# Performance work log

Hardware: AMD Instinct MI355X
Metric: run time of the kernel (lower is better)

The kernel has to match this reference:

```python
import jax, jax.numpy as jnp
import numpy as np

DIM = 1024
N_HEADS = 16
B, S = 2, 2048


def setup_inputs() -> dict:
    key = jax.random.key(0)
    ks = jax.random.split(key, 5)
    scale = 1.0 / np.sqrt(DIM)
    x = jax.random.normal(ks[0], (B, S, DIM), dtype=jnp.float32)
    mask = jax.random.randint(ks[1], (B, S), 0, 2, dtype=jnp.int32)
    Wq = jax.random.normal(ks[2], (DIM, DIM), dtype=jnp.float32) * scale
    Wk = jax.random.normal(ks[3], (DIM, DIM), dtype=jnp.float32) * scale
    Wv = jax.random.normal(ks[4], (DIM, DIM), dtype=jnp.float32) * scale
    bq = jnp.zeros((DIM,), jnp.float32)
    bk = jnp.zeros((DIM,), jnp.float32)
    bv = jnp.zeros((DIM,), jnp.float32)
    return {"x": x, "mask": mask, "Wq": Wq, "bq": bq, "Wk": Wk, "bk": bk, "Wv": Wv, "bv": bv}


def reference(x, mask, Wq, bq, Wk, bk, Wv, bv):
    # x: (B,S,D); project to q,k,v then split heads: (B,H,S,Dh)
    H = N_HEADS
    Bn, Sn, D = x.shape
    Dh = D // H

    def heads(t):
        return t.reshape(Bn, Sn, H, Dh).transpose(0, 2, 1, 3)

    q = heads(x @ Wq + bq)
    k = heads(x @ Wk + bk)
    v = heads(x @ Wv + bv)

    scores = jnp.einsum("bhsd,bhtd->bhst", q, k) / jnp.sqrt(jnp.float32(Dh))
    m = mask.astype(jnp.float32)[:, None, None, :]  # (B,1,1,S)
    scores = scores - 10000.0 * (1.0 - m)
    attn = jax.nn.softmax(scores, axis=-1)  # dropout is identity at eval (p=0)
    h = jnp.einsum("bhst,bhtd->bhsd", attn, v)
    return h.transpose(0, 2, 1, 3).reshape(Bn, Sn, D)
```

## Files before the change

### kernel.cpp

```cpp
#include <hip/hip_runtime.h>
#include <math.h>

#define DIMD 1024
#define NH 16
#define DH 64
#define BB 2
#define SS 2048
#define M_TOTAL (BB * SS)

typedef _Float16 half8 __attribute__((ext_vector_type(8)));
typedef _Float16 half4v __attribute__((ext_vector_type(4)));
typedef __fp16 fp16x2 __attribute__((ext_vector_type(2)));
typedef float floatx4 __attribute__((ext_vector_type(4)));
typedef float floatx16 __attribute__((ext_vector_type(16)));

#define QSCALE 0.18033688011112042f

__device__ __forceinline__ void load16_to_lds(const void* g, void* l) {
    __builtin_amdgcn_global_load_lds(
        (const __attribute__((address_space(1))) void*)g,
        (__attribute__((address_space(3))) void*)l, 16, 0, 0);
}

__device__ __forceinline__ unsigned pkh(float a, float b) {
    union { fp16x2 h; unsigned u; } c;
    c.h = __builtin_amdgcn_cvt_pkrtz(a, b);
    return c.u;
}

__global__ __launch_bounds__(256) void prep_kernel(
    const float* __restrict__ x,
    const float* __restrict__ Wq, const float* __restrict__ Wk,
    const float* __restrict__ Wv, const int* __restrict__ mask,
    _Float16* __restrict__ xh, _Float16* __restrict__ Wt,
    int* __restrict__ pos, int* __restrict__ nvalid)
{
    __shared__ _Float16 Ls[64][74];
    __shared__ int cnt[32], off[32];
    const int bid = blockIdx.x, tid = threadIdx.x;

    if (bid < 1024) {
#pragma unroll
        for (int j = 0; j < 4; ++j) {
            const int i = j * 262144 + bid * 256 + tid;
            float4 v = ((const float4*)x)[i];
            half4v hv = {(_Float16)v.x, (_Float16)v.y, (_Float16)v.z, (_Float16)v.w};
            *(half4v*)&xh[(size_t)i * 4] = hv;
        }
    } else if (bid < 1792) {
        const int wid = bid - 1024;
        const int z = wid >> 8, rem = wid & 255;
        const float* W = z == 0 ? Wq : (z == 1 ? Wk : Wv);
        _Float16* o = Wt + (size_t)z * DIMD * DIMD;
        const int k0 = (rem >> 4) * 64, n0 = (rem & 15) * 64;

#pragma unroll
        for (int it = 0; it < 4; ++it) {
            const int k = it * 16 + (tid >> 4);
            const int n4 = (tid & 15) * 4;
            float4 v = *(const float4*)&W[(size_t)(k0 + k) * DIMD + n0 + n4];
            Ls[k][n4 + 0] = (_Float16)v.x;
            Ls[k][n4 + 1] = (_Float16)v.y;
            Ls[k][n4 + 2] = (_Float16)v.z;
            Ls[k][n4 + 3] = (_Float16)v.w;
        }
        __syncthreads();
#pragma unroll
        for (int it = 0; it < 2; ++it) {
            const int idx = it * 256 + tid;
            const int n = idx >> 3, kc = idx & 7;
            union { _Float16 h[8]; uint4 u4; } t;
#pragma unroll
            for (int j = 0; j < 8; ++j) t.h[j] = Ls[kc * 8 + j][n];
            *(uint4*)&o[(size_t)(n0 + n) * DIMD + k0 + kc * 8] = t.u4;
        }
    } else {
        const int b = bid - 1792;
        const int wv = tid >> 6, lane = tid & 63;
        const unsigned long long lanemask = (lane == 63)
            ? 0x7fffffffffffffffull : ((1ull << lane) - 1ull);
        unsigned long long bms[8];
#pragma unroll
        for (int cc = 0; cc < 8; ++cc) {
            const int c = wv * 8 + cc;
            const int mv = mask[b * SS + c * 64 + lane];
            bms[cc] = __ballot(mv != 0);
            if (lane == 0) cnt[c] = __popcll(bms[cc]);
        }
        __syncthreads();
        if (tid == 0) {
            int s = 0;
            for (int c = 0; c < 32; ++c) { off[c] = s; s += cnt[c]; }
            nvalid[b] = s;
        }
        __syncthreads();
#pragma unroll
        for (int cc = 0; cc < 8; ++cc) {
            const int c = wv * 8 + cc;
            const int valid = (int)((bms[cc] >> lane) & 1ull);
            pos[b * SS + c * 64 + lane] =
                valid ? (off[c] + __popcll(bms[cc] & lanemask)) : -1;
        }
    }
}

__global__ __launch_bounds__(256) void proj_gemm(
    const _Float16* __restrict__ xh, const _Float16* __restrict__ Wt,
    const float* __restrict__ bq, const float* __restrict__ bk,
    const float* __restrict__ bv, const int* __restrict__ pos,
    _Float16* __restrict__ Q, _Float16* __restrict__ K, _Float16* __restrict__ Vt)
{
    const int z = blockIdx.z;
    const float* bias = z == 0 ? bq : (z == 1 ? bk : bv);
    const _Float16* Wz = Wt + (size_t)z * DIMD * DIMD;

    const _Float16* Aptr; const _Float16* Bptr; int m0, n0;
    if (z == 2) { Aptr = Wz; Bptr = xh; m0 = blockIdx.y * 128; n0 = blockIdx.x * 128; }
    else        { Aptr = xh; Bptr = Wz; m0 = blockIdx.x * 128; n0 = blockIdx.y * 128; }

    __shared__ _Float16 Ah[128 * 64];
    __shared__ _Float16 Bh[128 * 64];

    const int tid = threadIdx.x;
    const int wave = tid >> 6, lane = tid & 63;
    const int quad = lane >> 4, l16 = lane & 15;
    const int wm = (wave >> 1) * 64, wn = (wave & 1) * 64;
    const int sw = l16 & 7;

    const int tid8 = tid >> 3;
    const int gc = (tid & 7) ^ (tid8 & 7);
    const _Float16* ap = Aptr + (size_t)(m0 + tid8) * DIMD + gc * 8;
    const _Float16* bp = Bptr + (size_t)(n0 + tid8) * DIMD + gc * 8;
    const size_t RS = (size_t)32 * DIMD;
    _Float16* AhW = &Ah[(size_t)tid * 8];
    _Float16* BhW = &Bh[(size_t)tid * 8];

    floatx4 acc[4][4];
#pragma unroll
    for (int i = 0; i < 4; ++i)
#pragma unroll
        for (int j = 0; j < 4; ++j) acc[i][j] = (floatx4){0.f, 0.f, 0.f, 0.f};

    uint4 a0, a1, a2, a3, b0, b1, b2, b3;
    a0 = *(const uint4*)(ap);
    a1 = *(const uint4*)(ap + RS);
    a2 = *(const uint4*)(ap + 2 * RS);
    a3 = *(const uint4*)(ap + 3 * RS);
    b0 = *(const uint4*)(bp);
    b1 = *(const uint4*)(bp + RS);
    b2 = *(const uint4*)(bp + 2 * RS);
    b3 = *(const uint4*)(bp + 3 * RS);

    for (int kt = 0; kt < 16; ++kt) {
        *(uint4*)(AhW)        = a0;
        *(uint4*)(AhW + 2048) = a1;
        *(uint4*)(AhW + 4096) = a2;
        *(uint4*)(AhW + 6144) = a3;
        *(uint4*)(BhW)        = b0;
        *(uint4*)(BhW + 2048) = b1;
        *(uint4*)(BhW + 4096) = b2;
        *(uint4*)(BhW + 6144) = b3;

        if (kt < 15) {
            const _Float16* apk = ap + (kt + 1) * 64;
            const _Float16* bpk = bp + (kt + 1) * 64;
            a0 = *(const uint4*)(apk);
            a1 = *(const uint4*)(apk + RS);
            a2 = *(const uint4*)(apk + 2 * RS);
            a3 = *(const uint4*)(apk + 3 * RS);
            b0 = *(const uint4*)(bpk);
            b1 = *(const uint4*)(bpk + RS);
            b2 = *(const uint4*)(bpk + 2 * RS);
            b3 = *(const uint4*)(bpk + 3 * RS);
        }

        __syncthreads();

#pragma unroll
        for (int kc = 0; kc < 2; ++kc) {
            const int coff = ((quad + kc * 4) ^ sw) * 8;
            half8 af[4], bf[4];
#pragma unroll
            for (int mt = 0; mt < 4; ++mt)
                af[mt] = *(const half8*)&Ah[(wm + mt * 16 + l16) * 64 + coff];
#pragma unroll
            for (int nt = 0; nt < 4; ++nt)
                bf[nt] = *(const half8*)&Bh[(wn + nt * 16 + l16) * 64 + coff];
#pragma unroll
            for (int mt = 0; mt < 4; ++mt)
#pragma unroll
                for (int nt = 0; nt < 4; ++nt)
                    acc[mt][nt] = __builtin_amdgcn_mfma_f32_16x16x32_f16(
                        af[mt], bf[nt], acc[mt][nt], 0, 0, 0);
        }

        __syncthreads();
    }

    if (z < 2) {
        int prr[4][4];
#pragma unroll
        for (int mt = 0; mt < 4; ++mt)
#pragma unroll
            for (int r = 0; r < 4; ++r) {
                const int m = m0 + wm + mt * 16 + quad * 4 + r;
                prr[mt][r] = (z == 0) ? (m & 2047) : pos[m];
            }
#pragma unroll
        for (int nt = 0; nt < 4; ++nt) {
            const int n = n0 + wn + nt * 16 + l16;
            const float bn = bias[n];
            const int h = n >> 6, d = n & 63;
#pragma unroll
            for (int mt = 0; mt < 4; ++mt) {
#pragma unroll
                for (int r = 0; r < 4; ++r) {
                    if (prr[mt][r] < 0) continue;
                    const int m = m0 + wm + mt * 16 + quad * 4 + r;
                    const int b = m >> 11;
                    const _Float16 val = (_Float16)((acc[mt][nt][r] + bn) *
                                                    (z == 0 ? QSCALE : 1.0f));
                    _Float16* dst = (z == 0) ? Q : K;
                    dst[((((size_t)b * NH + h) * SS + prr[mt][r]) << 6) + d] = val;
                }
            }
        }
    } else {
#pragma unroll
        for (int nt = 0; nt < 4; ++nt) {
            const int gs = n0 + wn + nt * 16 + l16;
            const int prn = pos[gs];
            const int b = gs >> 11;
#pragma unroll
            for (int mt = 0; mt < 4; ++mt) {
#pragma unroll
                for (int r = 0; r < 4; ++r) {
                    if (prn < 0) continue;
                    const int drow = m0 + wm + mt * 16 + quad * 4 + r;
                    const int h = drow >> 6, dh = drow & 63;
                    Vt[(((size_t)b * NH + h) * DH + dh) * SS + prn] =
                        (_Float16)(acc[mt][nt][r] + bias[drow]);
                }
            }
        }
    }
}

__global__ __launch_bounds__(256, 2) void attn_kernel(
    const _Float16* __restrict__ Q, const _Float16* __restrict__ K,
    const _Float16* __restrict__ Vt, const int* __restrict__ nvalid,
    float* __restrict__ out)
{
    __shared__ __align__(16) char smem[34816];
    const int bid = blockIdx.x;
    const int bh = bid & 31;
    const int qt = bid >> 5;
    const int b = bh >> 4, h = bh & 15;
    const int q0 = qt * 128;
    const int tid = threadIdx.x, wave = tid >> 6, lane = tid & 63;
    const int hi = lane >> 5, l31 = lane & 31;

    const _Float16* Qb = Q + (size_t)bh * SS * DH;
    const _Float16* Kb = K + (size_t)bh * SS * DH;
    const _Float16* Vtb = Vt + (size_t)bh * DH * SS;

    const int nv = nvalid[b];
    const int ntiles = (nv + 63) >> 6;

    half8 qf[4];
#pragma unroll
    for (int ks = 0; ks < 4; ++ks)
        qf[ks] = *(const half8*)&Qb[(size_t)(q0 + wave * 32 + l31) * DH
                                    + ks * 16 + hi * 8];

#pragma unroll
    for (int it = 0; it < 2; ++it) {
        const int u = it * 256 + tid;
        const int row = u >> 3, gc = (u & 7) ^ (row & 7);
        load16_to_lds(&Kb[(size_t)row * DH + gc * 8],
                      (_Float16*)smem + (size_t)(it * 256 + wave * 64) * 8);
    }
#pragma unroll
    for (int it = 0; it < 2; ++it) {
        const int u = it * 256 + tid;
        const int row = u >> 3, gc = (u & 7) ^ (row & 7);
        load16_to_lds(&Vtb[(size_t)row * SS + gc * 8],
                      (_Float16*)(smem + 16384) + (size_t)(it * 256 + wave * 64) * 8);
    }
    __syncthreads();

    floatx16 O0, O1;
#pragma unroll
    for (int r = 0; r < 16; ++r) { O0[r] = 0.f; O1[r] = 0.f; }
    float l = 0.f;

    for (int i = 0; i < ntiles; ++i) {
        const int buf = i & 1;
        const int t0 = i * 64;

        if (i + 1 < ntiles) {
            const int nb = buf ^ 1, nt0 = t0 + 64;
            _Float16* KsN = (_Float16*)(smem + nb * 8192);
#pragma unroll
            for (int it = 0; it < 2; ++it) {
                const int u = it * 256 + tid;
                const int row = u >> 3, gc = (u & 7) ^ (row & 7);
                load16_to_lds(&Kb[(size_t)(nt0 + row) * DH + gc * 8],
                              KsN + (size_t)(it * 256 + wave * 64) * 8);
            }
            _Float16* VtN = (_Float16*)(smem + 16384 + nb * 8192);
#pragma unroll
            for (int it = 0; it < 2; ++it) {
                const int u = it * 256 + tid;
                const int row = u >> 3, gc = (u & 7) ^ (row & 7);
                load16_to_lds(&Vtb[(size_t)row * SS + nt0 + gc * 8],
                              VtN + (size_t)(it * 256 + wave * 64) * 8);
            }
        }

        const _Float16* KsB = (const _Float16*)(smem + buf * 8192);
        const _Float16* VtB = (const _Float16*)(smem + 16384 + buf * 8192);

        floatx16 S0, S1;
#pragma unroll
        for (int r = 0; r < 16; ++r) { S0[r] = 0.f; S1[r] = 0.f; }
#pragma unroll
        for (int ks = 0; ks < 4; ++ks) {
            const int c = 2 * ks + hi;
            const int r0 = l31, r1 = 32 + l31;
            half8 a0 = *(const half8*)&KsB[r0 * 64 + ((c ^ (r0 & 7)) << 3)];
            half8 a1 = *(const half8*)&KsB[r1 * 64 + ((c ^ (r1 & 7)) << 3)];
            S0 = __builtin_amdgcn_mfma_f32_32x32x16_f16(a0, qf[ks], S0, 0, 0, 0);
            S1 = __builtin_amdgcn_mfma_f32_32x32x16_f16(a1, qf[ks], S1, 0, 0, 0);
        }

        float p0[16], p1[16];
        if (t0 + 64 > nv) {
#pragma unroll
            for (int r = 0; r < 16; ++r) {
                const int tr = (r & 3) + 8 * (r >> 2) + 4 * hi;
                p0[r] = (t0 + tr < nv) ? exp2f(S0[r]) : 0.f;
                p1[r] = (t0 + 32 + tr < nv) ? exp2f(S1[r]) : 0.f;
            }
        } else {
#pragma unroll
            for (int r = 0; r < 16; ++r) {
                p0[r] = exp2f(S0[r]);
                p1[r] = exp2f(S1[r]);
            }
        }
#pragma unroll
        for (int r = 0; r < 16; ++r) l += p0[r] + p1[r];

        unsigned int pk0[8], pk1[8];
#pragma unroll
        for (int j = 0; j < 8; ++j) {
            pk0[j] = pkh(p0[2 * j], p0[2 * j + 1]);
            pk1[j] = pkh(p1[2 * j], p1[2 * j + 1]);
        }

#pragma unroll
        for (int ks = 0; ks < 4; ++ks) {
            const int k1 = ks & 1;
            const unsigned int* pk = (ks < 2) ? pk0 : pk1;
            const unsigned int a0 = pk[4 * k1 + 0], a1 = pk[4 * k1 + 1];
            const unsigned int b0 = pk[4 * k1 + 2], b1 = pk[4 * k1 + 3];
            const unsigned int s0 = hi ? a0 : b0, s1 = hi ? a1 : b1;
            const unsigned int r0v = __shfl_xor(s0, 32);
            const unsigned int r1v = __shfl_xor(s1, 32);
            union { unsigned int u[4]; half8 hv; } bfu;
            bfu.u[0] = hi ? r0v : a0;
            bfu.u[1] = hi ? r1v : a1;
            bfu.u[2] = hi ? b0 : r0v;
            bfu.u[3] = hi ? b1 : r1v;
            const int c = 2 * ks + hi;
            const int rd0 = l31, rd1 = 32 + l31;
            half8 v0 = *(const half8*)&VtB[rd0 * 64 + ((c ^ (rd0 & 7)) << 3)];
            half8 v1 = *(const half8*)&VtB[rd1 * 64 + ((c ^ (rd1 & 7)) << 3)];
            O0 = __builtin_amdgcn_mfma_f32_32x32x16_f16(v0, bfu.hv, O0, 0, 0, 0);
            O1 = __builtin_amdgcn_mfma_f32_32x32x16_f16(v1, bfu.hv, O1, 0, 0, 0);
        }

        __syncthreads();
    }

    l += __shfl_xor(l, 32);
    const float inv = 1.f / l;
    float* Ob = (float*)smem + wave * (32 * 68);
#pragma unroll
    for (int r = 0; r < 16; ++r) {
        const int dbase = (r & 3) + 8 * (r >> 2) + 4 * hi;
        Ob[l31 * 68 + dbase] = O0[r] * inv;
        Ob[l31 * 68 + 32 + dbase] = O1[r] * inv;
    }
    __syncthreads();

    const int qq = lane >> 1, part = lane & 1;
    float* op = out + ((size_t)(b * SS + q0 + wave * 32 + qq)) * DIMD
              + h * DH + part * 32;
#pragma unroll
    for (int j = 0; j < 8; ++j)
        *(float4*)&op[j * 4] = *(const float4*)&Ob[qq * 68 + part * 32 + j * 4];
}

extern "C" void kernel_launch(void* const* d_in, const int* in_sizes, int n_in,
                              void* d_out, int out_size, void* d_ws, size_t ws_size,
                              hipStream_t stream) {
    const float* x  = (const float*)d_in[0];
    const int* mask = (const int*)d_in[1];
    const float* Wq = (const float*)d_in[2];
    const float* bq = (const float*)d_in[3];
    const float* Wk = (const float*)d_in[4];
    const float* bk = (const float*)d_in[5];
    const float* Wv = (const float*)d_in[6];
    const float* bv = (const float*)d_in[7];
    float* out = (float*)d_out;

    _Float16* xh = (_Float16*)d_ws;
    _Float16* Wt = xh + (size_t)M_TOTAL * DIMD;
    _Float16* Q  = Wt + (size_t)3 * DIMD * DIMD;
    _Float16* K  = Q + (size_t)M_TOTAL * DIMD;
    _Float16* Vt = K + (size_t)M_TOTAL * DIMD;
    int* pos     = (int*)(Vt + (size_t)M_TOTAL * DIMD);
    int* nvalid  = pos + M_TOTAL;

    prep_kernel<<<1794, 256, 0, stream>>>(x, Wq, Wk, Wv, mask, xh, Wt, pos, nvalid);
    proj_gemm<<<dim3(32, 8, 3), 256, 0, stream>>>(
        xh, Wt, bq, bk, bv, pos, Q, K, Vt);
    attn_kernel<<<512, 256, 0, stream>>>(Q, K, Vt, nvalid, out);
}
```

Baseline: 173.0 us.

## Split KV tiles across two wave groups per attention block and merge partials

Doubles the attention block to 512 threads: two groups of four waves process alternating KV tiles for the same 128 queries, each with its own double-buffered K/Vt LDS region. Each group's row sums go through LDS to form the combined normalizer. Each group writes its normalized partial O to LDS, and all threads then sum the two partials and store coalesced rows. This aims to raise the wave count per CU and halve each wave's serial KV loop, at the cost of about double the LDS per block and an extra reduction step. When the tile count is odd, one group does a redundant, masked final tile.

```diff
diff --git a/kernel.cpp b/kernel.cpp
--- a/kernel.cpp
+++ b/kernel.cpp
@@ -246,18 +246,22 @@
     }
 }
 
-__global__ __launch_bounds__(256, 2) void attn_kernel(
+__global__ __launch_bounds__(512, 4) void attn_kernel(
     const _Float16* __restrict__ Q, const _Float16* __restrict__ K,
     const _Float16* __restrict__ Vt, const int* __restrict__ nvalid,
     float* __restrict__ out)
 {
-    __shared__ __align__(16) char smem[34816];
+    __shared__ __align__(16) char smem[70656];
     const int bid = blockIdx.x;
     const int bh = bid & 31;
     const int qt = bid >> 5;
     const int b = bh >> 4, h = bh & 15;
     const int q0 = qt * 128;
-    const int tid = threadIdx.x, wave = tid >> 6, lane = tid & 63;
+    const int tid = threadIdx.x;
+    const int lane = tid & 63;
+    const int grp = tid >> 8;
+    const int tidg = tid & 255;
+    const int wv4 = (tid >> 6) & 3;
     const int hi = lane >> 5, l31 = lane & 31;
 
     const _Float16* Qb = Q + (size_t)bh * SS * DH;
@@ -266,26 +270,33 @@
 
     const int nv = nvalid[b];
     const int ntiles = (nv + 63) >> 6;
+    const int nt2 = (ntiles + 1) >> 1;
+
+    char* gsm = smem + grp * 32768;
 
     half8 qf[4];
 #pragma unroll
     for (int ks = 0; ks < 4; ++ks)
-        qf[ks] = *(const half8*)&Qb[(size_t)(q0 + wave * 32 + l31) * DH
+        qf[ks] = *(const half8*)&Qb[(size_t)(q0 + wv4 * 32 + l31) * DH
                                     + ks * 16 + hi * 8];
 
-#pragma unroll
-    for (int it = 0; it < 2; ++it) {
-        const int u = it * 256 + tid;
-        const int row = u >> 3, gc = (u & 7) ^ (row & 7);
-        load16_to_lds(&Kb[(size_t)row * DH + gc * 8],
-                      (_Float16*)smem + (size_t)(it * 256 + wave * 64) * 8);
-    }
-#pragma unroll
-    for (int it = 0; it < 2; ++it) {
-        const int u = it * 256 + tid;
-        const int row = u >> 3, gc = (u & 7) ^ (row & 7);
-        load16_to_lds(&Vtb[(size_t)row * SS + gc * 8],
-                      (_Float16*)(smem + 16384) + (size_t)(it * 256 + wave * 64) * 8);
+    {
+        const int t = grp;
+        const int t0L = (t < ntiles) ? t * 64 : 0;
+#pragma unroll
+        for (int it = 0; it < 2; ++it) {
+            const int u = it * 256 + tidg;
+            const int row = u >> 3, gcs = (u & 7) ^ (row & 7);
+            load16_to_lds(&Kb[(size_t)(t0L + row) * DH + gcs * 8],
+                          (_Float16*)gsm + (size_t)(it * 256 + wv4 * 64) * 8);
+        }
+#pragma unroll
+        for (int it = 0; it < 2; ++it) {
+            const int u = it * 256 + tidg;
+            const int row = u >> 3, gcs = (u & 7) ^ (row & 7);
+            load16_to_lds(&Vtb[(size_t)row * SS + t0L + gcs * 8],
+                          (_Float16*)(gsm + 16384) + (size_t)(it * 256 + wv4 * 64) * 8);
+        }
     }
     __syncthreads();
 
@@ -294,32 +305,35 @@
     for (int r = 0; r < 16; ++r) { O0[r] = 0.f; O1[r] = 0.f; }
     float l = 0.f;
 
-    for (int i = 0; i < ntiles; ++i) {
+    for (int i = 0; i < nt2; ++i) {
         const int buf = i & 1;
-        const int t0 = i * 64;
-
-        if (i + 1 < ntiles) {
-            const int nb = buf ^ 1, nt0 = t0 + 64;
-            _Float16* KsN = (_Float16*)(smem + nb * 8192);
+        const int t = 2 * i + grp;
+        const int t0 = t * 64;
+
+        if (i + 1 < nt2) {
+            const int nb = buf ^ 1;
+            const int tn = t + 2;
+            const int nt0 = (tn < ntiles) ? tn * 64 : 0;
+            _Float16* KsN = (_Float16*)(gsm + nb * 8192);
 #pragma unroll
             for (int it = 0; it < 2; ++it) {
-                const int u = it * 256 + tid;
-                const int row = u >> 3, gc = (u & 7) ^ (row & 7);
-                load16_to_lds(&Kb[(size_t)(nt0 + row) * DH + gc * 8],
-                              KsN + (size_t)(it * 256 + wave * 64) * 8);
-            }
-            _Float16* VtN = (_Float16*)(smem + 16384 + nb * 8192);
+                const int u = it * 256 + tidg;
+                const int row = u >> 3, gcs = (u & 7) ^ (row & 7);
+                load16_to_lds(&Kb[(size_t)(nt0 + row) * DH + gcs * 8],
+                              KsN + (size_t)(it * 256 + wv4 * 64) * 8);
+            }
+            _Float16* VtN = (_Float16*)(gsm + 16384 + nb * 8192);
 #pragma unroll
             for (int it = 0; it < 2; ++it) {
-                const int u = it * 256 + tid;
-                const int row = u >> 3, gc = (u & 7) ^ (row & 7);
-                load16_to_lds(&Vtb[(size_t)row * SS + nt0 + gc * 8],
-                              VtN + (size_t)(it * 256 + wave * 64) * 8);
-            }
-        }
-
-        const _Float16* KsB = (const _Float16*)(smem + buf * 8192);
-        const _Float16* VtB = (const _Float16*)(smem + 16384 + buf * 8192);
+                const int u = it * 256 + tidg;
+                const int row = u >> 3, gcs = (u & 7) ^ (row & 7);
+                load16_to_lds(&Vtb[(size_t)row * SS + nt0 + gcs * 8],
+                              VtN + (size_t)(it * 256 + wv4 * 64) * 8);
+            }
+        }
+
+        const _Float16* KsB = (const _Float16*)(gsm + buf * 8192);
+        const _Float16* VtB = (const _Float16*)(gsm + 16384 + buf * 8192);
 
         floatx16 S0, S1;
 #pragma unroll
@@ -384,23 +398,34 @@
         __syncthreads();
     }
 
-    l += __shfl_xor(l, 32);
-    const float inv = 1.f / l;
-    float* Ob = (float*)smem + wave * (32 * 68);
+    float* labuf = (float*)(smem + 69632);
+    float lg = l + __shfl_xor(l, 32);
+    if (hi == 0) labuf[grp * 128 + wv4 * 32 + l31] = lg;
+    __syncthreads();
+
+    const float ltot = labuf[wv4 * 32 + l31] + labuf[128 + wv4 * 32 + l31];
+    const float inv = 1.f / ltot;
+    float* Obg = (float*)(smem + grp * 34816) + wv4 * (32 * 68);
 #pragma unroll
     for (int r = 0; r < 16; ++r) {
         const int dbase = (r & 3) + 8 * (r >> 2) + 4 * hi;
-        Ob[l31 * 68 + dbase] = O0[r] * inv;
-        Ob[l31 * 68 + 32 + dbase] = O1[r] * inv;
+        Obg[l31 * 68 + dbase] = O0[r] * inv;
+        Obg[l31 * 68 + 32 + dbase] = O1[r] * inv;
     }
     __syncthreads();
 
-    const int qq = lane >> 1, part = lane & 1;
-    float* op = out + ((size_t)(b * SS + q0 + wave * 32 + qq)) * DIMD
-              + h * DH + part * 32;
-#pragma unroll
-    for (int j = 0; j < 8; ++j)
-        *(float4*)&op[j * 4] = *(const float4*)&Ob[qq * 68 + part * 32 + j * 4];
+    const float* Ob0f = (const float*)smem;
+    const float* Ob1f = (const float*)(smem + 34816);
+#pragma unroll
+    for (int j = 0; j < 4; ++j) {
+        const int idx = j * 512 + tid;
+        const int q = idx >> 4, c4 = idx & 15;
+        const int off = (q >> 5) * (32 * 68) + (q & 31) * 68 + c4 * 4;
+        float4 a = *(const float4*)&Ob0f[off];
+        float4 c = *(const float4*)&Ob1f[off];
+        float4 s = {a.x + c.x, a.y + c.y, a.z + c.z, a.w + c.w};
+        *(float4*)&out[((size_t)(b * SS + q0 + q)) * DIMD + h * DH + c4 * 4] = s;
+    }
 }
 
 extern "C" void kernel_launch(void* const* d_in, const int* in_sizes, int n_in,
@@ -427,5 +452,5 @@
     prep_kernel<<<1794, 256, 0, stream>>>(x, Wq, Wk, Wv, mask, xh, Wt, pos, nvalid);
     proj_gemm<<<dim3(32, 8, 3), 256, 0, stream>>>(
         xh, Wt, bq, bk, bv, pos, Q, K, Vt);
-    attn_kernel<<<512, 256, 0, stream>>>(Q, K, Vt, nvalid, out);
-}
+    attn_kernel<<<512, 512, 0, stream>>>(Q, K, Vt, nvalid, out);
+}
```

Result: slower. 182.8 us (+5.6%).
